# Performance work log

Hardware: AMD Instinct MI355X
Metric: run time of the kernel (lower is better)

## Reference

```python
import jax, jax.numpy as jnp
import numpy as np
from math import pi

# Layer dims for num_inputs=0, width=64, depth=5, num_outputs=3
CHANNELS = [4, 64, 64, 64, 64, 3]

def _splits():
    biases, weights, idx = [], [], 0
    for l in range(len(CHANNELS) - 1):
        nci, nco = CHANNELS[l], CHANNELS[l + 1]
        biases.append((idx, idx + nco)); idx += nco
        weights.append((idx, idx + nci * nco)); idx += nci * nco
    return biases, weights, idx

BIASES, WEIGHTS, NUM_PARAMS = _splits()  # NUM_PARAMS == 12995


def _get_coords(h, w, ds):
    """Faithful port of _get_coords, including the original's bug where the
    y-channels reuse the normalized x coordinate vector (requires h == w)."""
    scale = 7.0 / 8.0
    x = jnp.arange(w, dtype=jnp.float32)
    y = jnp.arange(h, dtype=jnp.float32)
    x_c = (jnp.remainder(x, ds) / ds)
    y_c = (jnp.remainder(y, ds) / ds)
    x_c = x_c / (x_c.max() / scale)          # x_cos == x_sin in original
    y_cn = x_c / (y_c.max() / scale)          # bug: built from x_c
    xcos = jnp.cos(2.0 * pi * x_c)
    xsin = jnp.sin(2.0 * pi * x_c)
    ycos = jnp.cos(2.0 * pi * y_cn)           # length w, laid out along h (h==w)
    ysin = jnp.sin(2.0 * pi * y_cn)
    row = lambda v: jnp.broadcast_to(v[None, :], (h, w))
    col = lambda v: jnp.broadcast_to(v[:, None], (h, w))
    return jnp.stack([row(xcos), row(xsin), col(ycos), col(ysin)], axis=0)  # (4,h,w)


def setup_inputs() -> dict:
    key = jax.random.key(0)
    k1, k2 = jax.random.split(key)
    highres = jax.random.normal(k1, (2, 4, 512, 512), dtype=jnp.float32)
    lr_params = jax.random.normal(k2, (2, NUM_PARAMS, 64, 64), dtype=jnp.float32)
    return {"highres": highres, "lr_params": lr_params}


def reference(highres, lr_params):
    bs, _, h, w = highres.shape
    h_lr, w_lr = lr_params.shape[2], lr_params.shape[3]
    k = h // h_lr  # tile size

    coords = _get_coords(h, w, k)                       # (4, h, w)
    pe = jnp.broadcast_to(coords[None], (bs, 4, h, w))  # highres is overwritten by PE

    # unfold into (bs, h_lr, w_lr, k*k, 4) tiles
    tiles = pe.reshape(bs, 4, h_lr, k, w_lr, k)
    tiles = tiles.transpose(0, 2, 4, 3, 5, 1).reshape(bs, h_lr, w_lr, k * k, 4)

    out = tiles
    num_layers = len(CHANNELS) - 1
    for idx in range(num_layers):
        nci, nco = CHANNELS[idx], CHANNELS[idx + 1]
        b0, b1 = BIASES[idx]
        w0, w1 = WEIGHTS[idx]
        w_ = lr_params[:, w0:w1].transpose(0, 2, 3, 1).reshape(bs, h_lr, w_lr, nci, nco)
        b_ = lr_params[:, b0:b1].transpose(0, 2, 3, 1)[:, :, :, None, :]  # (bs,h_lr,w_lr,1,nco)
        out = jnp.einsum('bhwpi,bhwio->bhwpo', out, w_) + b_
        if idx < num_layers - 1:
            out = jnp.where(out >= 0, out, 0.01 * out)  # leaky_relu(0.01)
        else:
            out = jnp.tanh(out)

    out = out.reshape(bs, h_lr, w_lr, k, k, CHANNELS[-1])
    out = out.transpose(0, 5, 1, 3, 2, 4).reshape(bs, CHANNELS[-1], h, w)
    return out
```

## Files before the change

### kernel.cpp

```cpp
#include <hip/hip_runtime.h>
#include <math.h>


static constexpr int PLANE = 4096;
static constexpr int NPAR  = 12995;
static constexpr int AHI   = 8192;

__device__ __forceinline__ float leaky(float v) { return fmaxf(v, 0.01f * v); }

__device__ __forceinline__ constexpr float cx(int k) {
  constexpr float R = 0.70710678118654752f;
  const float t[8] = {1.f, R, 0.f, -R, -1.f, -R, 0.f, R};
  return t[k];
}
__device__ __forceinline__ constexpr float sx(int k) {
  constexpr float R = 0.70710678118654752f;
  const float t[8] = {0.f, R, 1.f, R, 0.f, -R, -1.f, -R};
  return t[k];
}

__global__ __launch_bounds__(256, 1) void pqn(const float* __restrict__ lr,
                                              float* __restrict__ out) {
  __shared__ alignas(16) float A[2 * AHI];
  __shared__ alignas(16) float WB[2][2048];

  const int tid = threadIdx.x;
  const int j   = tid & 3;
  const int pg  = (tid >> 2) & 7;
  const int cob = tid >> 5;

  const int n  = blockIdx.x;
  const int e2 = (n >> 3) & 3;
  const int P  = (n & 7) | ((n >> 5) << 3);
  const int jg = ((P & 3) << 2) | e2;
  const int i  = (P >> 2) & 63;
  const int b  = (P >> 8) & 1;

  const float* __restrict__ wb =
      lr + (size_t)b * NPAR * PLANE + (size_t)(i * 64 + jg * 4);
  const float* __restrict__ pt = wb + j;

  float fyc, fys;
  sincosf(0.78539816339744830962f * pg, &fys, &fyc);

  const int abase = pg * 16 + j * 4;
  const int swz   = j * 4;
  const int sq    = tid >> 7;
  const int sc    = tid & 127;

  auto gaddr = [&](int g) -> size_t {
    return 384 + (size_t)(g >> 3) * 4160 + (size_t)(g & 7) * 512;
  };

  float4 paA, paB;
  {
    const size_t cb = gaddr(0);
    paA = *(const float4*)(wb + (cb + tid) * PLANE);
    paB = *(const float4*)(wb + (cb + 256 + tid) * PLANE);
  }
  float l0b[8], l0w[32], bb[8];
#pragma unroll
  for (int m = 0; m < 8; ++m) l0b[m] = pt[(size_t)(cob * 8 + m) * PLANE];
#pragma unroll
  for (int f = 0; f < 4; ++f)
#pragma unroll
    for (int m = 0; m < 8; ++m)
      l0w[f * 8 + m] = pt[(size_t)(64 + f * 64 + cob * 8 + m) * PLANE];
#pragma unroll
  for (int m = 0; m < 8; ++m) bb[m] = pt[(size_t)(320 + cob * 8 + m) * PLANE];

#pragma unroll
  for (int col = 0; col < 8; ++col) {
    float t[8];
#pragma unroll
    for (int k = 0; k < 8; ++k) {
      float v = l0b[col];
      v = fmaf(cx(k), l0w[col], v);
      v = fmaf(sx(k), l0w[8 + col], v);
      v = fmaf(fyc,  l0w[16 + col], v);
      v = fmaf(fys,  l0w[24 + col], v);
      t[k] = leaky(v);
    }
    float4 v0, v1;
    v0.x = t[0]; v0.y = t[1]; v0.z = t[2]; v0.w = t[3];
    v1.x = t[4]; v1.y = t[5]; v1.z = t[6]; v1.w = t[7];
    *(float4*)&A[(cob * 8 + col) * 128 + abase]       = v0;
    *(float4*)&A[(cob * 8 + col) * 128 + abase + AHI] = v1;
  }
#pragma unroll
  for (int jj = 0; jj < 4; ++jj) {
    WB[0][sq * 512       + jj * 128 + (sc ^ (jj * 4))] = ((const float*)&paA)[jj];
    WB[0][(2 + sq) * 512 + jj * 128 + (sc ^ (jj * 4))] = ((const float*)&paB)[jj];
  }
  {
    const size_t cb = gaddr(1);
    paA = *(const float4*)(wb + (cb + tid) * PLANE);
    paB = *(const float4*)(wb + (cb + 256 + tid) * PLANE);
  }
  asm volatile("s_waitcnt lgkmcnt(0)" ::: "memory");
  __builtin_amdgcn_s_barrier();
  __builtin_amdgcn_sched_barrier(0);

  float y[64];
#pragma unroll
  for (int m = 0; m < 64; ++m) y[m] = 0.f;

  auto group = [&](int g, int h) {
    const float* WH = WB[h];
    const int r0 = (g & 7) * 8;
    float4 a0 = *(const float4*)&A[r0 * 128 + abase];
    float4 a1 = *(const float4*)&A[r0 * 128 + abase + AHI];
    float4 w0 = *(const float4*)&WH[j * 128 + ((cob * 8) ^ swz)];
    float4 w1 = *(const float4*)&WH[j * 128 + ((cob * 8 + 4) ^ swz)];
    __builtin_amdgcn_sched_barrier(0);
    if (g + 1 < 24) {
      float* WD = WB[h ^ 1];
#pragma unroll
      for (int jj = 0; jj < 4; ++jj) {
        WD[sq * 512       + jj * 128 + (sc ^ (jj * 4))] = ((const float*)&paA)[jj];
        WD[(2 + sq) * 512 + jj * 128 + (sc ^ (jj * 4))] = ((const float*)&paB)[jj];
      }
    }
    if (g + 2 < 24) {
      const size_t cb = gaddr(g + 2);
      paA = *(const float4*)(wb + (cb + tid) * PLANE);
      paB = *(const float4*)(wb + (cb + 256 + tid) * PLANE);
    }
    __builtin_amdgcn_sched_barrier(0);
#pragma unroll
    for (int t = 0; t < 8; ++t) {
      float4 na0, na1, nw0, nw1;
      if (t < 7) {
        const int tn = t + 1;
        const int ci = r0 + tn;
        const int q = tn >> 1, cl = tn & 1;
        na0 = *(const float4*)&A[ci * 128 + abase];
        na1 = *(const float4*)&A[ci * 128 + abase + AHI];
        nw0 = *(const float4*)&WH[q * 512 + j * 128 + ((cl * 64 + cob * 8) ^ swz)];
        nw1 = *(const float4*)&WH[q * 512 + j * 128 + ((cl * 64 + cob * 8 + 4) ^ swz)];
      }
      __builtin_amdgcn_sched_barrier(0);
      const float av[8] = {a0.x, a0.y, a0.z, a0.w, a1.x, a1.y, a1.z, a1.w};
      const float wv[8] = {w0.x, w0.y, w0.z, w0.w, w1.x, w1.y, w1.z, w1.w};
#pragma unroll
      for (int col = 0; col < 8; ++col)
#pragma unroll
        for (int k = 0; k < 8; ++k)
          y[col * 8 + k] = fmaf(av[k], wv[col], y[col * 8 + k]);
      if (t < 7) { a0 = na0; a1 = na1; w0 = nw0; w1 = nw1; }
    }
    asm volatile("s_waitcnt lgkmcnt(0)" ::: "memory");
    __builtin_amdgcn_s_barrier();
    __builtin_amdgcn_sched_barrier(0);
  };
  auto flush = [&](int l) {
#pragma unroll
    for (int col = 0; col < 8; ++col) {
      float4 v0, v1;
      v0.x = leaky(y[col * 8 + 0] + bb[col]);
      v0.y = leaky(y[col * 8 + 1] + bb[col]);
      v0.z = leaky(y[col * 8 + 2] + bb[col]);
      v0.w = leaky(y[col * 8 + 3] + bb[col]);
      v1.x = leaky(y[col * 8 + 4] + bb[col]);
      v1.y = leaky(y[col * 8 + 5] + bb[col]);
      v1.z = leaky(y[col * 8 + 6] + bb[col]);
      v1.w = leaky(y[col * 8 + 7] + bb[col]);
      *(float4*)&A[(cob * 8 + col) * 128 + abase]       = v0;
      *(float4*)&A[(cob * 8 + col) * 128 + abase + AHI] = v1;
    }
#pragma unroll
    for (int m = 0; m < 64; ++m) y[m] = 0.f;
    if (l < 2) {
#pragma unroll
      for (int m = 0; m < 8; ++m)
        bb[m] = pt[(size_t)(320 + (l + 1) * 4160 + cob * 8 + m) * PLANE];
    }
  };

#pragma unroll 1
  for (int u = 0; u < 12; ++u) {
    const int g0 = u * 2;
    group(g0, 0);
    const int g1 = g0 + 1;
    group(g1, 1);
    if ((g1 & 7) == 7) {
      flush(g1 >> 3);
      asm volatile("s_waitcnt lgkmcnt(0)" ::: "memory");
      __builtin_amdgcn_s_barrier();
      __builtin_amdgcn_sched_barrier(0);
    }
  }

  float po[24];
#pragma unroll
  for (int m = 0; m < 24; ++m) po[m] = 0.f;
#pragma unroll
  for (int cl = 0; cl < 8; ++cl) {
    const int ci = cob * 8 + cl;
    const float4 a0 = *(const float4*)&A[ci * 128 + abase];
    const float4 a1 = *(const float4*)&A[ci * 128 + abase + AHI];
#pragma unroll
    for (int o = 0; o < 3; ++o) {
      const float w = pt[(size_t)(12803 + ci * 3 + o) * PLANE];
      po[o * 8 + 0] = fmaf(a0.x, w, po[o * 8 + 0]);
      po[o * 8 + 1] = fmaf(a0.y, w, po[o * 8 + 1]);
      po[o * 8 + 2] = fmaf(a0.z, w, po[o * 8 + 2]);
      po[o * 8 + 3] = fmaf(a0.w, w, po[o * 8 + 3]);
      po[o * 8 + 4] = fmaf(a1.x, w, po[o * 8 + 4]);
      po[o * 8 + 5] = fmaf(a1.y, w, po[o * 8 + 5]);
      po[o * 8 + 6] = fmaf(a1.z, w, po[o * 8 + 6]);
      po[o * 8 + 7] = fmaf(a1.w, w, po[o * 8 + 7]);
    }
  }
  asm volatile("s_waitcnt lgkmcnt(0)" ::: "memory");
  __builtin_amdgcn_s_barrier();
  float* R = A;
#pragma unroll
  for (int m = 0; m < 24; m += 4)
    *(float4*)&R[tid * 28 + m] = *(float4*)&po[m];
  asm volatile("s_waitcnt lgkmcnt(0)" ::: "memory");
  __builtin_amdgcn_s_barrier();
  __builtin_amdgcn_sched_barrier(0);

  if (cob == 0) {
#pragma unroll
    for (int o = 0; o < 3; ++o) {
      const float bias = pt[(size_t)(12800 + o) * PLANE];
      float s[8];
#pragma unroll
      for (int k = 0; k < 8; ++k) s[k] = bias;
#pragma unroll
      for (int cb = 0; cb < 8; ++cb) {
#pragma unroll
        for (int k = 0; k < 8; ++k)
          s[k] += R[(cb * 32 + tid) * 28 + o * 8 + k];
      }
      float4 v0, v1;
      v0.x = tanhf(s[0]); v0.y = tanhf(s[1]); v0.z = tanhf(s[2]); v0.w = tanhf(s[3]);
      v1.x = tanhf(s[4]); v1.y = tanhf(s[5]); v1.z = tanhf(s[6]); v1.w = tanhf(s[7]);
      float* op = out + (size_t)b * 786432 + (size_t)o * 262144 +
                  (size_t)(i * 8 + pg) * 512 + (size_t)((jg * 4 + j) * 8);
      *(float4*)op = v0;
      *(float4*)(op + 4) = v1;
    }
  }
}

extern "C" void kernel_launch(void* const* d_in, const int* in_sizes, int n_in,
                              void* d_out, int out_size, void* d_ws, size_t ws_size,
                              hipStream_t stream) {
  (void)in_sizes; (void)n_in; (void)d_ws; (void)ws_size; (void)out_size;
  const float* lr = (const float*)d_in[1];
  float* out = (float*)d_out;
  hipLaunchKernelGGL(pqn, dim3(2048), dim3(256), 0, stream, lr, out);
}
```

Before: 246.6 us.

## Remap thread roles and swizzle LDS layouts; drop manual LDS prefetch

Threads are remapped so the pixel-group index varies fastest, then the output-channel block, then the column index. The activation buffer in shared memory is now XOR-swizzled by channel-block, and the staging layout for weight tiles is simplified so vectorised LDS reads avoid bank conflicts. The hand-written register double-buffering of LDS loads and the scheduling barriers inside the group loop are removed, leaving load/FMA interleaving to the compiler. This risks exposing more LDS latency in exchange for fewer bank conflicts and lower register pressure.

```diff
diff --git a/kernel.cpp b/kernel.cpp
--- a/kernel.cpp
+++ b/kernel.cpp
@@ -25,9 +25,9 @@
   __shared__ alignas(16) float WB[2][2048];
 
   const int tid = threadIdx.x;
-  const int j   = tid & 3;
-  const int pg  = (tid >> 2) & 7;
-  const int cob = tid >> 5;
+  const int pg  = tid & 7;
+  const int cob = (tid >> 3) & 7;
+  const int j   = tid >> 6;
 
   const int n  = blockIdx.x;
   const int e2 = (n >> 3) & 3;
@@ -43,10 +43,10 @@
   float fyc, fys;
   sincosf(0.78539816339744830962f * pg, &fys, &fyc);
 
-  const int abase = pg * 16 + j * 4;
-  const int swz   = j * 4;
-  const int sq    = tid >> 7;
-  const int sc    = tid & 127;
+  const int jrow = j * 32;
+  const int awr  = jrow + ((pg ^ cob) * 4);
+  const int wrd  = j * 128 + cob * 8;
+  const int pq0  = (tid >> 7) * 512 + ((tid >> 6) & 1) * 64 + (tid & 63);
 
   auto gaddr = [&](int g) -> size_t {
     return 384 + (size_t)(g >> 3) * 4160 + (size_t)(g & 7) * 512;
@@ -84,13 +84,13 @@
     float4 v0, v1;
     v0.x = t[0]; v0.y = t[1]; v0.z = t[2]; v0.w = t[3];
     v1.x = t[4]; v1.y = t[5]; v1.z = t[6]; v1.w = t[7];
-    *(float4*)&A[(cob * 8 + col) * 128 + abase]       = v0;
-    *(float4*)&A[(cob * 8 + col) * 128 + abase + AHI] = v1;
+    *(float4*)&A[(cob * 8 + col) * 128 + awr]       = v0;
+    *(float4*)&A[(cob * 8 + col) * 128 + awr + AHI] = v1;
   }
 #pragma unroll
   for (int jj = 0; jj < 4; ++jj) {
-    WB[0][sq * 512       + jj * 128 + (sc ^ (jj * 4))] = ((const float*)&paA)[jj];
-    WB[0][(2 + sq) * 512 + jj * 128 + (sc ^ (jj * 4))] = ((const float*)&paB)[jj];
+    WB[0][pq0 + jj * 128]        = ((const float*)&paA)[jj];
+    WB[0][pq0 + 1024 + jj * 128] = ((const float*)&paB)[jj];
   }
   {
     const size_t cb = gaddr(1);
@@ -106,19 +106,12 @@
   for (int m = 0; m < 64; ++m) y[m] = 0.f;
 
   auto group = [&](int g, int h) {
-    const float* WH = WB[h];
-    const int r0 = (g & 7) * 8;
-    float4 a0 = *(const float4*)&A[r0 * 128 + abase];
-    float4 a1 = *(const float4*)&A[r0 * 128 + abase + AHI];
-    float4 w0 = *(const float4*)&WH[j * 128 + ((cob * 8) ^ swz)];
-    float4 w1 = *(const float4*)&WH[j * 128 + ((cob * 8 + 4) ^ swz)];
-    __builtin_amdgcn_sched_barrier(0);
     if (g + 1 < 24) {
       float* WD = WB[h ^ 1];
 #pragma unroll
       for (int jj = 0; jj < 4; ++jj) {
-        WD[sq * 512       + jj * 128 + (sc ^ (jj * 4))] = ((const float*)&paA)[jj];
-        WD[(2 + sq) * 512 + jj * 128 + (sc ^ (jj * 4))] = ((const float*)&paB)[jj];
+        WD[pq0 + jj * 128]        = ((const float*)&paA)[jj];
+        WD[pq0 + 1024 + jj * 128] = ((const float*)&paB)[jj];
       }
     }
     if (g + 2 < 24) {
@@ -126,20 +119,17 @@
       paA = *(const float4*)(wb + (cb + tid) * PLANE);
       paB = *(const float4*)(wb + (cb + 256 + tid) * PLANE);
     }
-    __builtin_amdgcn_sched_barrier(0);
+    const float* WH = WB[h];
+    const int r0 = (g & 7) * 8;
+    const int aoff = jrow + ((pg ^ (g & 7)) * 4);
 #pragma unroll
     for (int t = 0; t < 8; ++t) {
-      float4 na0, na1, nw0, nw1;
-      if (t < 7) {
-        const int tn = t + 1;
-        const int ci = r0 + tn;
-        const int q = tn >> 1, cl = tn & 1;
-        na0 = *(const float4*)&A[ci * 128 + abase];
-        na1 = *(const float4*)&A[ci * 128 + abase + AHI];
-        nw0 = *(const float4*)&WH[q * 512 + j * 128 + ((cl * 64 + cob * 8) ^ swz)];
-        nw1 = *(const float4*)&WH[q * 512 + j * 128 + ((cl * 64 + cob * 8 + 4) ^ swz)];
-      }
-      __builtin_amdgcn_sched_barrier(0);
+      const int ci = r0 + t;
+      const int q = t >> 1, cl = t & 1;
+      const float4 a0 = *(const float4*)&A[ci * 128 + aoff];
+      const float4 a1 = *(const float4*)&A[ci * 128 + aoff + AHI];
+      const float4 w0 = *(const float4*)&WH[q * 512 + wrd + cl * 64];
+      const float4 w1 = *(const float4*)&WH[q * 512 + wrd + cl * 64 + 4];
       const float av[8] = {a0.x, a0.y, a0.z, a0.w, a1.x, a1.y, a1.z, a1.w};
       const float wv[8] = {w0.x, w0.y, w0.z, w0.w, w1.x, w1.y, w1.z, w1.w};
 #pragma unroll
@@ -147,7 +137,6 @@
 #pragma unroll
         for (int k = 0; k < 8; ++k)
           y[col * 8 + k] = fmaf(av[k], wv[col], y[col * 8 + k]);
-      if (t < 7) { a0 = na0; a1 = na1; w0 = nw0; w1 = nw1; }
     }
     asm volatile("s_waitcnt lgkmcnt(0)" ::: "memory");
     __builtin_amdgcn_s_barrier();
@@ -165,8 +154,8 @@
       v1.y = leaky(y[col * 8 + 5] + bb[col]);
       v1.z = leaky(y[col * 8 + 6] + bb[col]);
       v1.w = leaky(y[col * 8 + 7] + bb[col]);
-      *(float4*)&A[(cob * 8 + col) * 128 + abase]       = v0;
-      *(float4*)&A[(cob * 8 + col) * 128 + abase + AHI] = v1;
+      *(float4*)&A[(cob * 8 + col) * 128 + awr]       = v0;
+      *(float4*)&A[(cob * 8 + col) * 128 + awr + AHI] = v1;
     }
 #pragma unroll
     for (int m = 0; m < 64; ++m) y[m] = 0.f;
@@ -197,8 +186,8 @@
 #pragma unroll
   for (int cl = 0; cl < 8; ++cl) {
     const int ci = cob * 8 + cl;
-    const float4 a0 = *(const float4*)&A[ci * 128 + abase];
-    const float4 a1 = *(const float4*)&A[ci * 128 + abase + AHI];
+    const float4 a0 = *(const float4*)&A[ci * 128 + awr];
+    const float4 a1 = *(const float4*)&A[ci * 128 + awr + AHI];
 #pragma unroll
     for (int o = 0; o < 3; ++o) {
       const float w = pt[(size_t)(12803 + ci * 3 + o) * PLANE];
@@ -233,7 +222,7 @@
       for (int cb = 0; cb < 8; ++cb) {
 #pragma unroll
         for (int k = 0; k < 8; ++k)
-          s[k] += R[(cb * 32 + tid) * 28 + o * 8 + k];
+          s[k] += R[(tid + cb * 8) * 28 + o * 8 + k];
       }
       float4 v0, v1;
       v0.x = tanhf(s[0]); v0.y = tanhf(s[1]); v0.z = tanhf(s[2]); v0.w = tanhf(s[3]);
```

Result: no change. 250.3 us (+1.5%).

## Halve block to two tiles per workgroup, doubling grid and shrinking LDS

Applied to the files above, without the earlier changes.

Each workgroup now handles 2 low-res tiles with 128 threads instead of 4 tiles with 256 threads, and the grid doubles to 4096 blocks. The A activation buffer and weight staging buffers shrink by half. Global weight loads become float2 per plane instead of float4, and the XOR swizzle and sched_barriers in the inner loop are removed. The aim is more resident workgroups per CU and finer-grained scheduling, at the cost of narrower, less coalesced global loads and possible LDS bank conflicts without the swizzle.

```diff
diff --git a/kernel.cpp b/kernel.cpp
--- a/kernel.cpp
+++ b/kernel.cpp
@@ -4,7 +4,7 @@
 
 static constexpr int PLANE = 4096;
 static constexpr int NPAR  = 12995;
-static constexpr int AHI   = 8192;
+static constexpr int AHI   = 4096;
 
 __device__ __forceinline__ float leaky(float v) { return fmaxf(v, 0.01f * v); }
 
@@ -19,44 +19,44 @@
   return t[k];
 }
 
-__global__ __launch_bounds__(256, 1) void pqn(const float* __restrict__ lr,
+__global__ __launch_bounds__(128, 1) void pqn(const float* __restrict__ lr,
                                               float* __restrict__ out) {
   __shared__ alignas(16) float A[2 * AHI];
-  __shared__ alignas(16) float WB[2][2048];
+  __shared__ alignas(16) float WB[2][1024];
 
   const int tid = threadIdx.x;
-  const int j   = tid & 3;
-  const int pg  = (tid >> 2) & 7;
-  const int cob = tid >> 5;
+  const int j   = tid & 1;
+  const int pg  = (tid >> 1) & 7;
+  const int cob = tid >> 4;
 
   const int n  = blockIdx.x;
-  const int e2 = (n >> 3) & 3;
-  const int P  = (n & 7) | ((n >> 5) << 3);
-  const int jg = ((P & 3) << 2) | e2;
+  const int e3 = (n >> 3) & 7;
+  const int P  = (n & 7) | ((n >> 6) << 3);
+  const int jp = ((P & 3) << 3) | e3;
   const int i  = (P >> 2) & 63;
   const int b  = (P >> 8) & 1;
 
   const float* __restrict__ wb =
-      lr + (size_t)b * NPAR * PLANE + (size_t)(i * 64 + jg * 4);
+      lr + (size_t)b * NPAR * PLANE + (size_t)(i * 64 + jp * 2);
   const float* __restrict__ pt = wb + j;
 
   float fyc, fys;
   sincosf(0.78539816339744830962f * pg, &fys, &fyc);
 
-  const int abase = pg * 16 + j * 4;
-  const int swz   = j * 4;
-  const int sq    = tid >> 7;
-  const int sc    = tid & 127;
+  const int abase = pg * 8 + j * 4;
+  const int wrd   = j * 128 + cob * 8;
 
   auto gaddr = [&](int g) -> size_t {
     return 384 + (size_t)(g >> 3) * 4160 + (size_t)(g & 7) * 512;
   };
 
-  float4 paA, paB;
+  float2 pa0, pa1, pa2, pa3;
   {
     const size_t cb = gaddr(0);
-    paA = *(const float4*)(wb + (cb + tid) * PLANE);
-    paB = *(const float4*)(wb + (cb + 256 + tid) * PLANE);
+    pa0 = *(const float2*)(wb + (cb + tid) * PLANE);
+    pa1 = *(const float2*)(wb + (cb + 128 + tid) * PLANE);
+    pa2 = *(const float2*)(wb + (cb + 256 + tid) * PLANE);
+    pa3 = *(const float2*)(wb + (cb + 384 + tid) * PLANE);
   }
   float l0b[8], l0w[32], bb[8];
 #pragma unroll
@@ -84,19 +84,26 @@
     float4 v0, v1;
     v0.x = t[0]; v0.y = t[1]; v0.z = t[2]; v0.w = t[3];
     v1.x = t[4]; v1.y = t[5]; v1.z = t[6]; v1.w = t[7];
-    *(float4*)&A[(cob * 8 + col) * 128 + abase]       = v0;
-    *(float4*)&A[(cob * 8 + col) * 128 + abase + AHI] = v1;
-  }
-#pragma unroll
-  for (int jj = 0; jj < 4; ++jj) {
-    WB[0][sq * 512       + jj * 128 + (sc ^ (jj * 4))] = ((const float*)&paA)[jj];
-    WB[0][(2 + sq) * 512 + jj * 128 + (sc ^ (jj * 4))] = ((const float*)&paB)[jj];
-  }
-  {
-    const size_t cb = gaddr(1);
-    paA = *(const float4*)(wb + (cb + tid) * PLANE);
-    paB = *(const float4*)(wb + (cb + 256 + tid) * PLANE);
-  }
+    *(float4*)&A[(cob * 8 + col) * 64 + abase]       = v0;
+    *(float4*)&A[(cob * 8 + col) * 64 + abase + AHI] = v1;
+  }
+#define PUBLISH(WD)                                                            \
+  {                                                                            \
+    (WD)[tid]             = pa0.x; (WD)[128 + tid]       = pa0.y;              \
+    (WD)[256 + tid]       = pa1.x; (WD)[256 + 128 + tid] = pa1.y;              \
+    (WD)[512 + tid]       = pa2.x; (WD)[512 + 128 + tid] = pa2.y;              \
+    (WD)[768 + tid]       = pa3.x; (WD)[768 + 128 + tid] = pa3.y;              \
+  }
+#define REFILL(G)                                                              \
+  {                                                                            \
+    const size_t cb_ = gaddr(G);                                               \
+    pa0 = *(const float2*)(wb + (cb_ + tid) * PLANE);                          \
+    pa1 = *(const float2*)(wb + (cb_ + 128 + tid) * PLANE);                    \
+    pa2 = *(const float2*)(wb + (cb_ + 256 + tid) * PLANE);                    \
+    pa3 = *(const float2*)(wb + (cb_ + 384 + tid) * PLANE);                    \
+  }
+  PUBLISH(WB[0])
+  REFILL(1)
   asm volatile("s_waitcnt lgkmcnt(0)" ::: "memory");
   __builtin_amdgcn_s_barrier();
   __builtin_amdgcn_sched_barrier(0);
@@ -106,27 +113,14 @@
   for (int m = 0; m < 64; ++m) y[m] = 0.f;
 
   auto group = [&](int g, int h) {
+    if (g + 1 < 24) PUBLISH(WB[h ^ 1])
+    if (g + 2 < 24) REFILL(g + 2)
     const float* WH = WB[h];
+    float4 a0 = *(const float4*)&A[((g & 7) * 8) * 64 + abase];
+    float4 a1 = *(const float4*)&A[((g & 7) * 8) * 64 + abase + AHI];
+    float4 w0 = *(const float4*)&WH[wrd];
+    float4 w1 = *(const float4*)&WH[wrd + 4];
     const int r0 = (g & 7) * 8;
-    float4 a0 = *(const float4*)&A[r0 * 128 + abase];
-    float4 a1 = *(const float4*)&A[r0 * 128 + abase + AHI];
-    float4 w0 = *(const float4*)&WH[j * 128 + ((cob * 8) ^ swz)];
-    float4 w1 = *(const float4*)&WH[j * 128 + ((cob * 8 + 4) ^ swz)];
-    __builtin_amdgcn_sched_barrier(0);
-    if (g + 1 < 24) {
-      float* WD = WB[h ^ 1];
-#pragma unroll
-      for (int jj = 0; jj < 4; ++jj) {
-        WD[sq * 512       + jj * 128 + (sc ^ (jj * 4))] = ((const float*)&paA)[jj];
-        WD[(2 + sq) * 512 + jj * 128 + (sc ^ (jj * 4))] = ((const float*)&paB)[jj];
-      }
-    }
-    if (g + 2 < 24) {
-      const size_t cb = gaddr(g + 2);
-      paA = *(const float4*)(wb + (cb + tid) * PLANE);
-      paB = *(const float4*)(wb + (cb + 256 + tid) * PLANE);
-    }
-    __builtin_amdgcn_sched_barrier(0);
 #pragma unroll
     for (int t = 0; t < 8; ++t) {
       float4 na0, na1, nw0, nw1;
@@ -134,12 +128,11 @@
         const int tn = t + 1;
         const int ci = r0 + tn;
         const int q = tn >> 1, cl = tn & 1;
-        na0 = *(const float4*)&A[ci * 128 + abase];
-        na1 = *(const float4*)&A[ci * 128 + abase + AHI];
-        nw0 = *(const float4*)&WH[q * 512 + j * 128 + ((cl * 64 + cob * 8) ^ swz)];
-        nw1 = *(const float4*)&WH[q * 512 + j * 128 + ((cl * 64 + cob * 8 + 4) ^ swz)];
+        na0 = *(const float4*)&A[ci * 64 + abase];
+        na1 = *(const float4*)&A[ci * 64 + abase + AHI];
+        nw0 = *(const float4*)&WH[q * 256 + wrd + cl * 64];
+        nw1 = *(const float4*)&WH[q * 256 + wrd + cl * 64 + 4];
       }
-      __builtin_amdgcn_sched_barrier(0);
       const float av[8] = {a0.x, a0.y, a0.z, a0.w, a1.x, a1.y, a1.z, a1.w};
       const float wv[8] = {w0.x, w0.y, w0.z, w0.w, w1.x, w1.y, w1.z, w1.w};
 #pragma unroll
@@ -165,8 +158,8 @@
       v1.y = leaky(y[col * 8 + 5] + bb[col]);
       v1.z = leaky(y[col * 8 + 6] + bb[col]);
       v1.w = leaky(y[col * 8 + 7] + bb[col]);
-      *(float4*)&A[(cob * 8 + col) * 128 + abase]       = v0;
-      *(float4*)&A[(cob * 8 + col) * 128 + abase + AHI] = v1;
+      *(float4*)&A[(cob * 8 + col) * 64 + abase]       = v0;
+      *(float4*)&A[(cob * 8 + col) * 64 + abase + AHI] = v1;
     }
 #pragma unroll
     for (int m = 0; m < 64; ++m) y[m] = 0.f;
@@ -190,6 +183,8 @@
       __builtin_amdgcn_sched_barrier(0);
     }
   }
+#undef PUBLISH
+#undef REFILL
 
   float po[24];
 #pragma unroll
@@ -197,8 +192,8 @@
 #pragma unroll
   for (int cl = 0; cl < 8; ++cl) {
     const int ci = cob * 8 + cl;
-    const float4 a0 = *(const float4*)&A[ci * 128 + abase];
-    const float4 a1 = *(const float4*)&A[ci * 128 + abase + AHI];
+    const float4 a0 = *(const float4*)&A[ci * 64 + abase];
+    const float4 a1 = *(const float4*)&A[ci * 64 + abase + AHI];
 #pragma unroll
     for (int o = 0; o < 3; ++o) {
       const float w = pt[(size_t)(12803 + ci * 3 + o) * PLANE];
@@ -233,13 +228,13 @@
       for (int cb = 0; cb < 8; ++cb) {
 #pragma unroll
         for (int k = 0; k < 8; ++k)
-          s[k] += R[(cb * 32 + tid) * 28 + o * 8 + k];
+          s[k] += R[(tid + cb * 16) * 28 + o * 8 + k];
       }
       float4 v0, v1;
       v0.x = tanhf(s[0]); v0.y = tanhf(s[1]); v0.z = tanhf(s[2]); v0.w = tanhf(s[3]);
       v1.x = tanhf(s[4]); v1.y = tanhf(s[5]); v1.z = tanhf(s[6]); v1.w = tanhf(s[7]);
       float* op = out + (size_t)b * 786432 + (size_t)o * 262144 +
-                  (size_t)(i * 8 + pg) * 512 + (size_t)((jg * 4 + j) * 8);
+                  (size_t)(i * 8 + pg) * 512 + (size_t)((jp * 2 + j) * 8);
       *(float4*)op = v0;
       *(float4*)(op + 4) = v1;
     }
@@ -252,5 +247,5 @@
   (void)in_sizes; (void)n_in; (void)d_ws; (void)ws_size; (void)out_size;
   const float* lr = (const float*)d_in[1];
   float* out = (float*)d_out;
-  hipLaunchKernelGGL(pqn, dim3(2048), dim3(256), 0, stream, lr, out);
-}
+  hipLaunchKernelGGL(pqn, dim3(4096), dim3(128), 0, stream, lr, out);
+}
```

New measurement: 332.2 us. 34.7% more time.
